# Performance work log

Measured on AMD Instinct MI355X. Metric: run time of the kernel, lower is better.

## Reference

```python
import jax, jax.numpy as jnp
import numpy as np

HEADS = 16
DIM_HEAD = 64
SCALE = DIM_HEAD ** -0.5
EPS = 1e-5


def _bitlinear(x, w):
    """BitNet b1.58 BitLinear (kyegomez/BitNet), eval-mode, bias-free.
    w: [out, in] torch-layout. Ternary weight quant (scale = mean|w|),
    per-token int8 absmax activation quant, straight-through estimator.
    """
    ws = 1.0 / jnp.clip(jnp.mean(jnp.abs(w)), EPS, None)
    wq = jnp.clip(jnp.round(w * ws), -1.0, 1.0) / ws
    wq = w + jax.lax.stop_gradient(wq - w)
    xs = 127.0 / jnp.clip(jnp.max(jnp.abs(x), axis=-1, keepdims=True), EPS, None)
    xq = jnp.clip(jnp.round(x * xs), -128.0, 127.0) / xs
    xq = x + jax.lax.stop_gradient(xq - x)
    return jnp.einsum('bnd,od->bno', xq, wq)


def setup_inputs() -> dict:
    key = jax.random.key(0)
    ks = jax.random.split(key, 6)
    b, n, d = 2, 2048, 1024
    return {
        'x': jax.random.normal(ks[0], (b, n, d), dtype=jnp.float32),
        'context': jax.random.normal(ks[1], (b, n, d), dtype=jnp.float32),
        'Wq': jax.random.normal(ks[2], (d, d), dtype=jnp.float32) * 0.02,
        'Wk': jax.random.normal(ks[3], (d, d), dtype=jnp.float32) * 0.02,
        'Wv': jax.random.normal(ks[4], (d, d), dtype=jnp.float32) * 0.02,
        'Wo': jax.random.normal(ks[5], (d, d), dtype=jnp.float32) * 0.02,
    }


def reference(x, context, Wq, Wk, Wv, Wo):
    b, n, _ = x.shape
    m = context.shape[1]
    q = _bitlinear(x, Wq)
    k = _bitlinear(context, Wk)
    v = _bitlinear(context, Wv)
    # b n (h d) -> b h n d
    q = q.reshape(b, n, HEADS, DIM_HEAD).transpose(0, 2, 1, 3)
    k = k.reshape(b, m, HEADS, DIM_HEAD).transpose(0, 2, 1, 3)
    v = v.reshape(b, m, HEADS, DIM_HEAD).transpose(0, 2, 1, 3)
    dots = jnp.einsum('bhid,bhjd->bhij', q, k) * SCALE
    attn = jax.nn.softmax(dots, axis=-1)  # dropout is identity in eval
    out = jnp.einsum('bhij,bhjd->bhid', attn, v)
    out = out.transpose(0, 2, 1, 3).reshape(b, n, HEADS * DIM_HEAD)
    return _bitlinear(out, Wo)
```

## Files before the change

### kernel.cpp

```cpp
#include <hip/hip_runtime.h>
#include <math.h>

#define HEADS   16
#define DHEAD   64
#define SEQ     2048
#define NB      2
#define DM      1024
#define NTOK    4096
#define WEPS    1e-5

using f16x8   = __attribute__((ext_vector_type(8))) _Float16;
using f16x4   = __attribute__((ext_vector_type(4))) _Float16;
using fp16x2  = __attribute__((ext_vector_type(2))) __fp16;
using floatx4 = __attribute__((ext_vector_type(4))) float;
using i32x4   = __attribute__((ext_vector_type(4))) int;

typedef __attribute__((address_space(1))) unsigned int gu32;
typedef __attribute__((address_space(3))) unsigned int lu32;

#define BAR_LGKM()  asm volatile("s_waitcnt lgkmcnt(0)\n\ts_barrier" ::: "memory")
#define WAIT_LGKM() asm volatile("s_waitcnt lgkmcnt(0)" ::: "memory")

__device__ __forceinline__ unsigned short h16b(_Float16 h) {
    union { _Float16 h; unsigned short u; } c; c.h = h; return c.u;
}
__device__ __forceinline__ unsigned pk2u(fp16x2 v) {
    union { fp16x2 h; unsigned u; } c; c.h = v; return c.u;
}

__global__ void wsum1(const float* __restrict__ w0, const float* __restrict__ w1,
                      const float* __restrict__ w2, const float* __restrict__ w3,
                      double* __restrict__ partial) {
    const float* w = (blockIdx.y == 0) ? w0 : (blockIdx.y == 1) ? w1 : (blockIdx.y == 2) ? w2 : w3;
    int base = blockIdx.x * 16384;
    double s = 0.0;
    for (int i = threadIdx.x; i < 16384; i += 256)
        s += fabs((double)w[base + i]);
    __shared__ double sd[256];
    sd[threadIdx.x] = s;
    __syncthreads();
    for (int st = 128; st > 0; st >>= 1) {
        if (threadIdx.x < st) sd[threadIdx.x] += sd[threadIdx.x + st];
        __syncthreads();
    }
    if (threadIdx.x == 0) partial[blockIdx.y * 64 + blockIdx.x] = sd[0];
}

__global__ void wsum2(const double* __restrict__ partial, double* __restrict__ wscale) {
    int t = threadIdx.x;
    if (t < 4) {
        double s = 0.0;
        for (int i = 0; i < 64; i++) s += partial[t * 64 + i];
        double mean = s / (1024.0 * 1024.0);
        wscale[t] = (mean > WEPS) ? mean : WEPS;
    }
}

__global__ void wquant(const float* __restrict__ w0, const float* __restrict__ w1,
                       const float* __restrict__ w2, const float* __restrict__ w3,
                       const double* __restrict__ wscale, signed char* __restrict__ wq) {
    int widx = blockIdx.y;
    const float* w = (widx == 0) ? w0 : (widx == 1) ? w1 : (widx == 2) ? w2 : w3;
    double ws = 1.0 / wscale[widx];
    int idx = (blockIdx.x * 256 + threadIdx.x) * 4;
    float4 wv = *(const float4*)(w + idx);
    char4 o;
    {
        double r = rint((double)wv.x * ws); r = r > 1.0 ? 1.0 : (r < -1.0 ? -1.0 : r); o.x = (signed char)r;
    } {
        double r = rint((double)wv.y * ws); r = r > 1.0 ? 1.0 : (r < -1.0 ? -1.0 : r); o.y = (signed char)r;
    } {
        double r = rint((double)wv.z * ws); r = r > 1.0 ? 1.0 : (r < -1.0 ? -1.0 : r); o.z = (signed char)r;
    } {
        double r = rint((double)wv.w * ws); r = r > 1.0 ? 1.0 : (r < -1.0 ? -1.0 : r); o.w = (signed char)r;
    }
    *(char4*)(wq + (size_t)widx * 1048576 + idx) = o;
}

__device__ __forceinline__ void aquant_row(const float* __restrict__ row,
                                           signed char* __restrict__ dst_row,
                                           double* __restrict__ ascale_p) {
    int t = threadIdx.x;
    float4 xv = *(const float4*)(row + t * 4);
    float a = fmaxf(fmaxf(fabsf(xv.x), fabsf(xv.y)), fmaxf(fabsf(xv.z), fabsf(xv.w)));
    __shared__ float sm[256];
    sm[t] = a;
    __syncthreads();
    for (int st = 128; st > 0; st >>= 1) {
        if (t < st) sm[t] = fmaxf(sm[t], sm[t + st]);
        __syncthreads();
    }
    double mx = (double)sm[0];
    if (mx < WEPS) mx = WEPS;
    if (t == 0) *ascale_p = mx / 127.0;
    double xs = 127.0 / mx;
    char4 o;
    {
        double r = rint((double)xv.x * xs); r = r > 127.0 ? 127.0 : (r < -128.0 ? -128.0 : r); o.x = (signed char)r;
    } {
        double r = rint((double)xv.y * xs); r = r > 127.0 ? 127.0 : (r < -128.0 ? -128.0 : r); o.y = (signed char)r;
    } {
        double r = rint((double)xv.z * xs); r = r > 127.0 ? 127.0 : (r < -128.0 ? -128.0 : r); o.z = (signed char)r;
    } {
        double r = rint((double)xv.w * xs); r = r > 127.0 ? 127.0 : (r < -128.0 ? -128.0 : r); o.w = (signed char)r;
    }
    *(char4*)(dst_row + t * 4) = o;
}

__global__ void aquant(const float* __restrict__ src, signed char* __restrict__ dst,
                       double* __restrict__ ascale) {
    int tok = blockIdx.x;
    aquant_row(src + (size_t)tok * DM, dst + (size_t)tok * DM, ascale + tok);
}

__global__ void aquant2(const float* __restrict__ x, const float* __restrict__ ctx,
                        signed char* __restrict__ dst, double* __restrict__ ascale) {
    int tok = blockIdx.x;
    const float* row = (tok < NTOK) ? x + (size_t)tok * DM : ctx + (size_t)(tok - NTOK) * DM;
    aquant_row(row, dst + (size_t)tok * DM, ascale + tok);
}

__device__ __forceinline__ void gemm_core(
        const signed char* __restrict__ A, const signed char* __restrict__ W,
        const double* __restrict__ ascale, double wsc,
        void* __restrict__ outp, int mode, float prescale, int bx, int by) {
    __shared__ __align__(16) signed char lds_a[128 * 64];
    __shared__ __align__(16) signed char lds_b[128 * 64];
    const int tid  = threadIdx.x;
    const int wave = tid >> 6, lane = tid & 63;
    const int wr = wave >> 1, wc = wave & 1;
    const int quad = lane >> 4, l15 = lane & 15;
    const int row0 = by * 128, col0 = bx * 128;
    i32x4 acc[4][4] = {};

    const signed char* ga0 = A + (size_t)(row0 + (lane >> 2)) * DM + (lane & 3) * 16;
    const signed char* gb0 = W + (size_t)(col0 + (lane >> 2)) * DM + (lane & 3) * 16;

    for (int k0 = 0; k0 < DM; k0 += 64) {
        __syncthreads();
        #pragma unroll
        for (int t = 0; t < 2; t++) {
            const int i = wave + t * 4;
            __builtin_amdgcn_global_load_lds(
                (const gu32*)(const void*)(ga0 + (size_t)i * 16 * DM + k0),
                (lu32*)(void*)(lds_a + i * 1024), 16, 0, 0);
            __builtin_amdgcn_global_load_lds(
                (const gu32*)(const void*)(gb0 + (size_t)i * 16 * DM + k0),
                (lu32*)(void*)(lds_b + i * 1024), 16, 0, 0);
        }
        __syncthreads();
        i32x4 af[4], bfr[4];
        #pragma unroll
        for (int mi = 0; mi < 4; mi++) {
            int r = wr * 64 + mi * 16 + l15;
            af[mi] = *(const i32x4*)&lds_a[r * 64 + quad * 16];
        }
        #pragma unroll
        for (int ni = 0; ni < 4; ni++) {
            int n = wc * 64 + ni * 16 + l15;
            bfr[ni] = *(const i32x4*)&lds_b[n * 64 + quad * 16];
        }
        #pragma unroll
        for (int mi = 0; mi < 4; mi++)
            #pragma unroll
            for (int ni = 0; ni < 4; ni++)
                acc[mi][ni] = __builtin_amdgcn_mfma_i32_16x16x64_i8(af[mi], bfr[ni], acc[mi][ni], 0, 0, 0);
    }

    #pragma unroll
    for (int mi = 0; mi < 4; mi++) {
        int tbase = row0 + wr * 64 + mi * 16 + quad * 4;
        if (mode == 2) {
            int bb = tbase >> 11, n = tbase & 2047;
            int tile = n >> 5, tin = n & 31;
            #pragma unroll
            for (int ni = 0; ni < 4; ni++) {
                int o = col0 + wc * 64 + ni * 16 + l15;
                int hh = o >> 6, dh = o & 63;
                ushort4 hv, lv;
                #pragma unroll
                for (int reg = 0; reg < 4; reg++) {
                    double sa = ascale[tbase + reg] * wsc;
                    float fv = (float)((double)acc[mi][ni][reg] * sa) * prescale;
                    _Float16 hl = (_Float16)fv;
                    _Float16 ml = (_Float16)((fv - (float)hl) * 2048.0f);
                    ((unsigned short*)&hv)[reg] = h16b(hl);
                    ((unsigned short*)&lv)[reg] = h16b(ml);
                }
                size_t idx = (((size_t)(bb * HEADS + hh) * 64 + tile) * 64 + dh) * 32 + tin;
                *(ushort4*)((unsigned short*)outp + idx)           = hv;
                *(ushort4*)((unsigned short*)outp + idx + 4194304) = lv;
            }
        } else {
            #pragma unroll
            for (int reg = 0; reg < 4; reg++) {
                int t = tbase + reg;
                double sa = ascale[t] * wsc;
                #pragma unroll
                for (int ni = 0; ni < 4; ni++) {
                    int o = col0 + wc * 64 + ni * 16 + l15;
                    float val = (float)((double)acc[mi][ni][reg] * sa);
                    if (mode == 1) {
                        ((float*)outp)[(size_t)t * DM + o] = val;
                    } else {
                        int bb = t >> 11, n = t & 2047, hh = o >> 6, dh = o & 63;
                        float fv = val * prescale;
                        _Float16 hl = (_Float16)fv;
                        _Float16 ml = (_Float16)((fv - (float)hl) * 2048.0f);
                        size_t idx = (((size_t)(bb * HEADS + hh) * SEQ + n) << 6) + dh;
                        ((unsigned short*)outp)[idx]           = h16b(hl);
                        ((unsigned short*)outp)[idx + 4194304] = h16b(ml);
                    }
                }
            }
        }
    }
}

__global__ __launch_bounds__(256) void gemm_qkv(
        const signed char* __restrict__ xq, const signed char* __restrict__ cq,
        const signed char* __restrict__ wqb, const double* __restrict__ ascale_x,
        const double* __restrict__ wscale, void* __restrict__ qkv) {
    const int which = blockIdx.x >> 3;
    char* base = (char*)qkv + (size_t)which * 16777216;
    gemm_core(which == 0 ? xq : cq,
              wqb + (size_t)which * 1048576,
              ascale_x + (which ? NTOK : 0),
              wscale[which],
              base,
              which == 2 ? 2 : 0,
              which == 0 ? 0.18033688011112042f : 1.0f, blockIdx.x & 7, blockIdx.y);
}

__global__ __launch_bounds__(256) void gemm_o(
        const signed char* __restrict__ aq, const signed char* __restrict__ wo,
        const double* __restrict__ ascale, const double* __restrict__ wscale_p,
        float* __restrict__ out) {
    gemm_core(aq, wo, ascale, *wscale_p, out, 1, 1.0f, blockIdx.x, blockIdx.y);
}

#define KH_IDX(row, d8) (((row) * 8 + ((d8) ^ ((row) & 7))) * 8)

__global__ __launch_bounds__(256, 2) void attn_mfma(
        const unsigned short* __restrict__ qhg, const unsigned short* __restrict__ qlg,
        const unsigned short* __restrict__ khg, const unsigned short* __restrict__ klg,
        const unsigned short* __restrict__ vhg, const unsigned short* __restrict__ vlg,
        float* __restrict__ out) {
    __shared__ __align__(16) _Float16 KhL[32 * 64];
    __shared__ __align__(16) _Float16 KlL[32 * 64];
    __shared__ __align__(16) _Float16 PhL[4][32 * 36];
    __shared__ __align__(16) _Float16 PlL[4][32 * 36];
    __shared__ float Lp[4][2][16][4];

    const int lin  = blockIdx.x;
    const int bh   = (lin & 7) * 4 + ((lin >> 3) & 3);
    const int qblk = lin >> 5;
    const int tid  = threadIdx.x;
    const int wave = tid >> 6, lane = tid & 63;
    const int l15  = lane & 15, quad = lane >> 4;
    const int qbase = qblk * 128 + wave * 32;

    f16x8 qh[2][2], qm[2][2];
    #pragma unroll
    for (int qs = 0; qs < 2; qs++) {
        #pragma unroll
        for (int c = 0; c < 2; c++) {
            size_t off = (((size_t)bh * SEQ + qbase + qs * 16 + l15) << 6) + c * 32 + quad * 8;
            qh[qs][c] = *(const f16x8*)(qhg + off);
            qm[qs][c] = *(const f16x8*)(qlg + off);
        }
    }

    floatx4 och[2][4] = {};
    floatx4 ocm[2][4] = {};
    float lsum[2] = {0.f, 0.f};
    const floatx4 zf = {};

    const unsigned short* khb = khg + ((size_t)bh * SEQ << 6);
    const unsigned short* klb = klg + ((size_t)bh * SEQ << 6);
    const unsigned short* vhb = vhg + ((size_t)bh << 17);
    const unsigned short* vlb = vlg + ((size_t)bh << 17);

    const int kk = tid >> 3, d8 = tid & 7;

    uint4 kh_pf = *(const uint4*)(khb + ((size_t)kk << 6) + d8 * 8);
    uint4 kl_pf = *(const uint4*)(klb + ((size_t)kk << 6) + d8 * 8);
    f16x8 vfh[4], vfm[4];
    #pragma unroll
    for (int nh = 0; nh < 4; nh++) {
        size_t vo = ((size_t)(nh * 16 + l15) << 5) + quad * 8;
        vfh[nh] = *(const f16x8*)(vhb + vo);
        vfm[nh] = *(const f16x8*)(vlb + vo);
    }

    for (int t = 0; t < 64; t++) {
        BAR_LGKM();

        *(uint4*)&KhL[KH_IDX(kk, d8)] = kh_pf;
        *(uint4*)&KlL[KH_IDX(kk, d8)] = kl_pf;

        if (t + 1 < 64) {
            kh_pf = *(const uint4*)(khb + ((size_t)((t + 1) * 32 + kk) << 6) + d8 * 8);
            kl_pf = *(const uint4*)(klb + ((size_t)((t + 1) * 32 + kk) << 6) + d8 * 8);
        }

        BAR_LGKM();

        f16x8 kfh[2][2], kfl[2][2];
        #pragma unroll
        for (int ms = 0; ms < 2; ms++) {
            #pragma unroll
            for (int c = 0; c < 2; c++) {
                kfh[ms][c] = *(const f16x8*)&KhL[KH_IDX(ms * 16 + l15, c * 4 + quad)];
                kfl[ms][c] = *(const f16x8*)&KlL[KH_IDX(ms * 16 + l15, c * 4 + quad)];
            }
        }

        __builtin_amdgcn_s_setprio(1);
        floatx4 ah[2][2], am[2][2];
        #pragma unroll
        for (int qs = 0; qs < 2; qs++) {
            #pragma unroll
            for (int ms = 0; ms < 2; ms++) {
                ah[qs][ms] = __builtin_amdgcn_mfma_f32_16x16x32_f16(kfh[ms][0], qh[qs][0], zf, 0, 0, 0);
                am[qs][ms] = __builtin_amdgcn_mfma_f32_16x16x32_f16(kfh[ms][0], qm[qs][0], zf, 0, 0, 0);
                am[qs][ms] = __builtin_amdgcn_mfma_f32_16x16x32_f16(kfl[ms][0], qh[qs][0], am[qs][ms], 0, 0, 0);
                ah[qs][ms] = __builtin_amdgcn_mfma_f32_16x16x32_f16(kfh[ms][1], qh[qs][1], ah[qs][ms], 0, 0, 0);
                am[qs][ms] = __builtin_amdgcn_mfma_f32_16x16x32_f16(kfh[ms][1], qm[qs][1], am[qs][ms], 0, 0, 0);
                am[qs][ms] = __builtin_amdgcn_mfma_f32_16x16x32_f16(kfl[ms][1], qh[qs][1], am[qs][ms], 0, 0, 0);
            }
        }
        __builtin_amdgcn_s_setprio(0);

        #pragma unroll
        for (int qs = 0; qs < 2; qs++) {
            #pragma unroll
            for (int ms = 0; ms < 2; ms++) {
                float p0 = __builtin_amdgcn_exp2f(ah[qs][ms][0] + am[qs][ms][0] * 4.8828125e-4f);
                float p1 = __builtin_amdgcn_exp2f(ah[qs][ms][1] + am[qs][ms][1] * 4.8828125e-4f);
                float p2 = __builtin_amdgcn_exp2f(ah[qs][ms][2] + am[qs][ms][2] * 4.8828125e-4f);
                float p3 = __builtin_amdgcn_exp2f(ah[qs][ms][3] + am[qs][ms][3] * 4.8828125e-4f);
                lsum[qs] += (p0 + p1) + (p2 + p3);
                fp16x2 h01 = __builtin_amdgcn_cvt_pkrtz(p0, p1);
                fp16x2 h23 = __builtin_amdgcn_cvt_pkrtz(p2, p3);
                fp16x2 m01 = __builtin_amdgcn_cvt_pkrtz((p0 - (float)h01[0]) * 2048.0f,
                                                        (p1 - (float)h01[1]) * 2048.0f);
                fp16x2 m23 = __builtin_amdgcn_cvt_pkrtz((p2 - (float)h23[0]) * 2048.0f,
                                                        (p3 - (float)h23[1]) * 2048.0f);
                int poff = (qs * 16 + l15) * 36 + ms * 16 + quad * 4;
                *(uint2*)&PhL[wave][poff] = make_uint2(pk2u(h01), pk2u(h23));
                *(uint2*)&PlL[wave][poff] = make_uint2(pk2u(m01), pk2u(m23));
            }
        }
        WAIT_LGKM();

        __builtin_amdgcn_s_setprio(1);
        #pragma unroll
        for (int qs = 0; qs < 2; qs++) {
            f16x8 pfh = *(const f16x8*)&PhL[wave][(qs * 16 + l15) * 36 + quad * 8];
            f16x8 pfm = *(const f16x8*)&PlL[wave][(qs * 16 + l15) * 36 + quad * 8];
            #pragma unroll
            for (int nh = 0; nh < 4; nh++) {
                och[qs][nh] = __builtin_amdgcn_mfma_f32_16x16x32_f16(pfh, vfh[nh], och[qs][nh], 0, 0, 0);
                ocm[qs][nh] = __builtin_amdgcn_mfma_f32_16x16x32_f16(pfh, vfm[nh], ocm[qs][nh], 0, 0, 0);
                ocm[qs][nh] = __builtin_amdgcn_mfma_f32_16x16x32_f16(pfm, vfh[nh], ocm[qs][nh], 0, 0, 0);
            }
        }
        __builtin_amdgcn_s_setprio(0);

        if (t + 1 < 64) {
            #pragma unroll
            for (int nh = 0; nh < 4; nh++) {
                size_t vo = ((size_t)((t + 1) * 64 + nh * 16 + l15) << 5) + quad * 8;
                vfh[nh] = *(const f16x8*)(vhb + vo);
                vfm[nh] = *(const f16x8*)(vlb + vo);
            }
        }
    }

    Lp[wave][0][l15][quad] = lsum[0];
    Lp[wave][1][l15][quad] = lsum[1];
    WAIT_LGKM();

    int b = bh >> 4, h = bh & 15;
    #pragma unroll
    for (int qs = 0; qs < 2; qs++) {
        float linv[4];
        #pragma unroll
        for (int r = 0; r < 4; r++) {
            float4 lv = *(const float4*)&Lp[wave][qs][quad * 4 + r][0];
            linv[r] = 1.0f / (lv.x + lv.y + lv.z + lv.w);
        }
        #pragma unroll
        for (int nh = 0; nh < 4; nh++) {
            #pragma unroll
            for (int r = 0; r < 4; r++) {
                int token = b * SEQ + qbase + qs * 16 + quad * 4 + r;
                float val = (och[qs][nh][r] + ocm[qs][nh][r] * 4.8828125e-4f) * linv[r];
                out[(size_t)token * DM + h * 64 + nh * 16 + l15] = val;
            }
        }
    }
}

extern "C" void kernel_launch(void* const* d_in, const int* in_sizes, int n_in,
                              void* d_out, int out_size, void* d_ws, size_t ws_size,
                              hipStream_t stream) {
    const float* x       = (const float*)d_in[0];
    const float* context = (const float*)d_in[1];
    const float* Wq      = (const float*)d_in[2];
    const float* Wk      = (const float*)d_in[3];
    const float* Wv      = (const float*)d_in[4];
    const float* Wo      = (const float*)d_in[5];
    char* ws = (char*)d_ws;

    double* wscale   = (double*)(ws + 0);
    double* partial  = (double*)(ws + 4096);
    double* ascale_x = (double*)(ws + 8192);
    double* ascale_a = (double*)(ws + 73728);
    signed char* wqb = (signed char*)(ws + 131072);
    signed char* xq  = (signed char*)(ws + 4325376);
    signed char* cq  = (signed char*)(ws + 8519680);
    float* attn_out  = (float*)(ws + 4325376);
    char* planes     = ws + 21102592;
    signed char* aq  = (signed char*)(ws + 21102592);

    unsigned short* qhg = (unsigned short*)planes;
    unsigned short* qlg = qhg + 4194304;
    unsigned short* khg = (unsigned short*)(planes + 16777216);
    unsigned short* klg = khg + 4194304;
    unsigned short* vhg = (unsigned short*)(planes + 33554432);
    unsigned short* vlg = vhg + 4194304;

    wsum1<<<dim3(64, 4), 256, 0, stream>>>(Wq, Wk, Wv, Wo, partial);
    wsum2<<<1, 64, 0, stream>>>(partial, wscale);
    wquant<<<dim3(1024, 4), 256, 0, stream>>>(Wq, Wk, Wv, Wo, wscale, wqb);
    aquant2<<<2 * NTOK, 256, 0, stream>>>(x, context, xq, ascale_x);

    gemm_qkv<<<dim3(24, 32), 256, 0, stream>>>(xq, cq, wqb, ascale_x, wscale, planes);

    attn_mfma<<<dim3(512), 256, 0, stream>>>(qhg, qlg, khg, klg, vhg, vlg, attn_out);

    aquant<<<NTOK, 256, 0, stream>>>(attn_out, aq, ascale_a);
    gemm_o<<<dim3(8, 32), 256, 0, stream>>>(aq, wqb + 3145728, ascale_a, wscale + 3, (float*)d_out);
}
```

Baseline: 269.8 us.

## Split KV sequence across two wave groups per attention block and merge partials

The attention kernel launches 512-thread blocks where each half of the waves processes half of the key/value sequence for the same query tile. Partial row sums and output accumulators from the second half are reduced through shared memory by the first half before normalization and store. This halves the serial loop length per wave and raises wave-level parallelism, at the cost of larger shared memory per block, extra barriers and a reduction step.

```diff
diff --git a/kernel.cpp b/kernel.cpp
--- a/kernel.cpp
+++ b/kernel.cpp
@@ -241,24 +241,27 @@
 
 #define KH_IDX(row, d8) (((row) * 8 + ((d8) ^ ((row) & 7))) * 8)
 
-__global__ __launch_bounds__(256, 2) void attn_mfma(
+__global__ __launch_bounds__(512, 4) void attn_mfma(
         const unsigned short* __restrict__ qhg, const unsigned short* __restrict__ qlg,
         const unsigned short* __restrict__ khg, const unsigned short* __restrict__ klg,
         const unsigned short* __restrict__ vhg, const unsigned short* __restrict__ vlg,
         float* __restrict__ out) {
-    __shared__ __align__(16) _Float16 KhL[32 * 64];
-    __shared__ __align__(16) _Float16 KlL[32 * 64];
-    __shared__ __align__(16) _Float16 PhL[4][32 * 36];
-    __shared__ __align__(16) _Float16 PlL[4][32 * 36];
-    __shared__ float Lp[4][2][16][4];
+    __shared__ __align__(16) char smem[57344];
+    _Float16* KhL = (_Float16*)smem;
+    _Float16* KlL = (_Float16*)(smem + 8192);
+    _Float16* PhL = (_Float16*)(smem + 16384);
+    _Float16* PlL = (_Float16*)(smem + 34816);
+    float*    Lpf = (float*)(smem + 53248);
+    float*    Om  = (float*)(smem + 16384);
 
     const int lin  = blockIdx.x;
     const int bh   = (lin & 7) * 4 + ((lin >> 3) & 3);
-    const int qblk = lin >> 5;
+    const int qblk = (lin >> 5) & 15;
     const int tid  = threadIdx.x;
     const int wave = tid >> 6, lane = tid & 63;
+    const int whalf = wave >> 2, wsub = wave & 3;
     const int l15  = lane & 15, quad = lane >> 4;
-    const int qbase = qblk * 128 + wave * 32;
+    const int qbase = qblk * 128 + wsub * 32;
 
     f16x8 qh[2][2], qm[2][2];
     #pragma unroll
@@ -281,27 +284,30 @@
     const unsigned short* vhb = vhg + ((size_t)bh << 17);
     const unsigned short* vlb = vlg + ((size_t)bh << 17);
 
-    const int kk = tid >> 3, d8 = tid & 7;
-
-    uint4 kh_pf = *(const uint4*)(khb + ((size_t)kk << 6) + d8 * 8);
-    uint4 kl_pf = *(const uint4*)(klb + ((size_t)kk << 6) + d8 * 8);
+    const int kk = (tid >> 3) & 31, d8 = tid & 7;
+    const int kvbase = whalf * 1024;
+    _Float16* KhH = KhL + whalf * 2048;
+    _Float16* KlH = KlL + whalf * 2048;
+
+    uint4 kh_pf = *(const uint4*)(khb + ((size_t)(kvbase + kk) << 6) + d8 * 8);
+    uint4 kl_pf = *(const uint4*)(klb + ((size_t)(kvbase + kk) << 6) + d8 * 8);
     f16x8 vfh[4], vfm[4];
     #pragma unroll
     for (int nh = 0; nh < 4; nh++) {
-        size_t vo = ((size_t)(nh * 16 + l15) << 5) + quad * 8;
+        size_t vo = ((size_t)((whalf * 32) * 64 + nh * 16 + l15) << 5) + quad * 8;
         vfh[nh] = *(const f16x8*)(vhb + vo);
         vfm[nh] = *(const f16x8*)(vlb + vo);
     }
 
-    for (int t = 0; t < 64; t++) {
+    for (int t = 0; t < 32; t++) {
         BAR_LGKM();
 
-        *(uint4*)&KhL[KH_IDX(kk, d8)] = kh_pf;
-        *(uint4*)&KlL[KH_IDX(kk, d8)] = kl_pf;
-
-        if (t + 1 < 64) {
-            kh_pf = *(const uint4*)(khb + ((size_t)((t + 1) * 32 + kk) << 6) + d8 * 8);
-            kl_pf = *(const uint4*)(klb + ((size_t)((t + 1) * 32 + kk) << 6) + d8 * 8);
+        *(uint4*)&KhH[KH_IDX(kk, d8)] = kh_pf;
+        *(uint4*)&KlH[KH_IDX(kk, d8)] = kl_pf;
+
+        if (t + 1 < 32) {
+            kh_pf = *(const uint4*)(khb + ((size_t)(kvbase + (t + 1) * 32 + kk) << 6) + d8 * 8);
+            kl_pf = *(const uint4*)(klb + ((size_t)(kvbase + (t + 1) * 32 + kk) << 6) + d8 * 8);
         }
 
         BAR_LGKM();
@@ -311,8 +317,8 @@
         for (int ms = 0; ms < 2; ms++) {
             #pragma unroll
             for (int c = 0; c < 2; c++) {
-                kfh[ms][c] = *(const f16x8*)&KhL[KH_IDX(ms * 16 + l15, c * 4 + quad)];
-                kfl[ms][c] = *(const f16x8*)&KlL[KH_IDX(ms * 16 + l15, c * 4 + quad)];
+                kfh[ms][c] = *(const f16x8*)&KhH[KH_IDX(ms * 16 + l15, c * 4 + quad)];
+                kfl[ms][c] = *(const f16x8*)&KlH[KH_IDX(ms * 16 + l15, c * 4 + quad)];
             }
         }
 
@@ -347,9 +353,9 @@
                                                         (p1 - (float)h01[1]) * 2048.0f);
                 fp16x2 m23 = __builtin_amdgcn_cvt_pkrtz((p2 - (float)h23[0]) * 2048.0f,
                                                         (p3 - (float)h23[1]) * 2048.0f);
-                int poff = (qs * 16 + l15) * 36 + ms * 16 + quad * 4;
-                *(uint2*)&PhL[wave][poff] = make_uint2(pk2u(h01), pk2u(h23));
-                *(uint2*)&PlL[wave][poff] = make_uint2(pk2u(m01), pk2u(m23));
+                int poff = wave * 1152 + (qs * 16 + l15) * 36 + ms * 16 + quad * 4;
+                *(uint2*)&PhL[poff] = make_uint2(pk2u(h01), pk2u(h23));
+                *(uint2*)&PlL[poff] = make_uint2(pk2u(m01), pk2u(m23));
             }
         }
         WAIT_LGKM();
@@ -357,8 +363,8 @@
         __builtin_amdgcn_s_setprio(1);
         #pragma unroll
         for (int qs = 0; qs < 2; qs++) {
-            f16x8 pfh = *(const f16x8*)&PhL[wave][(qs * 16 + l15) * 36 + quad * 8];
-            f16x8 pfm = *(const f16x8*)&PlL[wave][(qs * 16 + l15) * 36 + quad * 8];
+            f16x8 pfh = *(const f16x8*)&PhL[wave * 1152 + (qs * 16 + l15) * 36 + quad * 8];
+            f16x8 pfm = *(const f16x8*)&PlL[wave * 1152 + (qs * 16 + l15) * 36 + quad * 8];
             #pragma unroll
             for (int nh = 0; nh < 4; nh++) {
                 och[qs][nh] = __builtin_amdgcn_mfma_f32_16x16x32_f16(pfh, vfh[nh], och[qs][nh], 0, 0, 0);
@@ -368,36 +374,52 @@
         }
         __builtin_amdgcn_s_setprio(0);
 
-        if (t + 1 < 64) {
+        if (t + 1 < 32) {
             #pragma unroll
             for (int nh = 0; nh < 4; nh++) {
-                size_t vo = ((size_t)((t + 1) * 64 + nh * 16 + l15) << 5) + quad * 8;
+                size_t vo = ((size_t)((whalf * 32 + t + 1) * 64 + nh * 16 + l15) << 5) + quad * 8;
                 vfh[nh] = *(const f16x8*)(vhb + vo);
                 vfm[nh] = *(const f16x8*)(vlb + vo);
             }
         }
     }
 
-    Lp[wave][0][l15][quad] = lsum[0];
-    Lp[wave][1][l15][quad] = lsum[1];
-    WAIT_LGKM();
-
-    int b = bh >> 4, h = bh & 15;
-    #pragma unroll
-    for (int qs = 0; qs < 2; qs++) {
-        float linv[4];
-        #pragma unroll
-        for (int r = 0; r < 4; r++) {
-            float4 lv = *(const float4*)&Lp[wave][qs][quad * 4 + r][0];
-            linv[r] = 1.0f / (lv.x + lv.y + lv.z + lv.w);
-        }
-        #pragma unroll
-        for (int nh = 0; nh < 4; nh++) {
+    Lpf[((wave * 2 + 0) * 16 + l15) * 4 + quad] = lsum[0];
+    Lpf[((wave * 2 + 1) * 16 + l15) * 4 + quad] = lsum[1];
+    __syncthreads();
+
+    if (whalf == 1) {
+        #pragma unroll
+        for (int qs = 0; qs < 2; qs++)
+            #pragma unroll
+            for (int nh = 0; nh < 4; nh++)
+                #pragma unroll
+                for (int r = 0; r < 4; r++)
+                    Om[((((wsub * 2 + qs) * 4 + nh) * 4 + r) << 6) + lane] =
+                        och[qs][nh][r] + ocm[qs][nh][r] * 4.8828125e-4f;
+    }
+    __syncthreads();
+
+    if (whalf == 0) {
+        int b = bh >> 4, h = bh & 15;
+        #pragma unroll
+        for (int qs = 0; qs < 2; qs++) {
+            float linv[4];
             #pragma unroll
             for (int r = 0; r < 4; r++) {
-                int token = b * SEQ + qbase + qs * 16 + quad * 4 + r;
-                float val = (och[qs][nh][r] + ocm[qs][nh][r] * 4.8828125e-4f) * linv[r];
-                out[(size_t)token * DM + h * 64 + nh * 16 + l15] = val;
+                float4 a = *(const float4*)&Lpf[((wave * 2 + qs) * 16 + quad * 4 + r) * 4];
+                float4 c = *(const float4*)&Lpf[(((wave + 4) * 2 + qs) * 16 + quad * 4 + r) * 4];
+                linv[r] = 1.0f / (a.x + a.y + a.z + a.w + c.x + c.y + c.z + c.w);
+            }
+            #pragma unroll
+            for (int nh = 0; nh < 4; nh++) {
+                #pragma unroll
+                for (int r = 0; r < 4; r++) {
+                    int token = b * SEQ + qbase + qs * 16 + quad * 4 + r;
+                    float val = (och[qs][nh][r] + ocm[qs][nh][r] * 4.8828125e-4f
+                                 + Om[((((wsub * 2 + qs) * 4 + nh) * 4 + r) << 6) + lane]) * linv[r];
+                    out[(size_t)token * DM + h * 64 + nh * 16 + l15] = val;
+                }
             }
         }
     }
@@ -439,7 +461,7 @@
 
     gemm_qkv<<<dim3(24, 32), 256, 0, stream>>>(xq, cq, wqb, ascale_x, wscale, planes);
 
-    attn_mfma<<<dim3(512), 256, 0, stream>>>(qhg, qlg, khg, klg, vhg, vlg, attn_out);
+    attn_mfma<<<dim3(512), 512, 0, stream>>>(qhg, qlg, khg, klg, vhg, vlg, attn_out);
 
     aquant<<<NTOK, 256, 0, stream>>>(attn_out, aq, ascale_a);
     gemm_o<<<dim3(8, 32), 256, 0, stream>>>(aq, wqb + 3145728, ascale_a, wscale + 3, (float*)d_out);
```

Result: slower. 899.8 us (+233.5%).
